# Optimization experiments

Hardware: AMD Instinct MI355X
Metric: run time of the kernel (lower is better)

The kernel has to match this reference:

```python
import jax, jax.numpy as jnp
from jax import lax
import numpy as np

B, T, UMAX, D = 32, 128, 64, 512
U1 = UMAX + 1
BLANK = D - 1  # blank=-1 -> last vocab slot
NEG = -1e30    # finite -inf surrogate (keeps logaddexp grads NaN-free)


def setup_inputs() -> dict:
    key = jax.random.key(0)
    k1, k2, k3, k4 = jax.random.split(key, 4)
    logits = jax.random.normal(k1, (B, T, U1, D), dtype=jnp.float32)
    logit_lengths = jax.random.randint(k2, (B,), T // 2, T + 1, dtype=jnp.int32)
    target_lengths = jax.random.randint(k3, (B,), UMAX // 2, UMAX + 1, dtype=jnp.int32)
    targets = jax.random.randint(k4, (B, UMAX), 0, D - 1, dtype=jnp.int32)  # never blank
    return {"logits": logits, "logit_lengths": logit_lengths,
            "target_lengths": target_lengths, "targets": targets}


def _transducer_costs(log_probs, logit_lengths, target_lengths, targets):
    """RNN-T alpha DP; costs[b] = -(alpha[T_b-1, U_b] + lp_blank[T_b-1, U_b])."""
    b, t_max, u1, d = log_probs.shape
    lp_blank = log_probs[..., BLANK]                                   # [B,T,U1]
    tgt_pad = jnp.concatenate([targets, jnp.zeros((b, 1), targets.dtype)], axis=1)  # [B,U1]
    lp_emit = jnp.take_along_axis(log_probs, tgt_pad[:, None, :, None], axis=3)[..., 0]  # [B,T,U1]
    u_idx = jnp.arange(u1)
    # emit transitions only exist for u < target_length (masks padded labels too)
    lp_emit = jnp.where(u_idx[None, None, :] < target_lengths[:, None, None], lp_emit, NEG)

    # alpha[0, u] = cumsum of emit log-probs along u
    row0 = jnp.concatenate(
        [jnp.zeros((b, 1), jnp.float32), jnp.cumsum(lp_emit[:, 0, :-1], axis=1)], axis=1)

    def row_step(prev_row, xs):
        lpb_prev, lpe = xs                      # both [B,U1]
        skip = prev_row + lpb_prev              # alpha[t-1,u] + blank(t-1,u)

        def inner(a_left, xu):
            s_u, e_um1 = xu                      # skip[:,u], lp_emit[:,t,u-1]
            a = jnp.logaddexp(s_u, a_left + e_um1)
            return a, a

        a0 = skip[:, 0]
        _, rest = lax.scan(inner, a0,
                           (jnp.moveaxis(skip[:, 1:], 1, 0),
                            jnp.moveaxis(lpe[:, :-1], 1, 0)))
        row = jnp.concatenate([a0[:, None], jnp.moveaxis(rest, 0, 1)], axis=1)
        return row, row

    xs = (jnp.moveaxis(lp_blank[:, :-1, :], 1, 0),   # blank at row t-1
          jnp.moveaxis(lp_emit[:, 1:, :], 1, 0))     # emit at row t
    _, rows = lax.scan(row_step, row0, xs)
    alpha = jnp.concatenate([row0[:, None, :], jnp.moveaxis(rows, 0, 1)], axis=1)  # [B,T,U1]

    bi = jnp.arange(b)
    tf = logit_lengths - 1
    uf = target_lengths
    return -(alpha[bi, tf, uf] + lp_blank[bi, tf, uf])


def reference(logits, logit_lengths, target_lengths, targets):
    lp = jax.nn.log_softmax(logits, axis=-1)
    return _transducer_costs(lp, logit_lengths, target_lengths, targets)
```

## Files before the change

### kernel.cpp

```cpp
#include <hip/hip_runtime.h>

#define BQ 32
#define TQ 128
#define U1Q 65
#define UMAXQ 64
#define DQ 512
#define SLAB (TQ * U1Q)
#define NCELLS (BQ * SLAB)
#define NEGQ (-1e30f)
#define L2E 1.4426950408889634f
#define LN2F 0.6931471805599453f

typedef float f4 __attribute__((ext_vector_type(4)));

__device__ __forceinline__ float logadd2(float x, float y) {
    float mx = fmaxf(x, y);
    float d  = fminf(x, y) - mx;
    return mx + log2f(1.0f + exp2f(d));
}

__global__ __launch_bounds__(512) void lse_k(const float* __restrict__ logits,
                                             const int* __restrict__ targets,
                                             const int* __restrict__ llen,
                                             const int* __restrict__ tlen,
                                             float* __restrict__ ws) {
    int wid  = (blockIdx.x * 512 + threadIdx.x) >> 6;
    int lane = threadIdx.x & 63;
    int g = lane >> 4;
    int i = lane & 15;
    int r = wid * 4 + g;

    int b = r / SLAB;
    int q = r - b * SLAB;
    int t = q / U1Q;
    int u = q - t * U1Q;
    int tl = tlen[b];
    if (t >= llen[b] || u > tl) return;

    const f4* rp = (const f4*)(logits + (size_t)r * DQ) + i;
    f4 v0 = __builtin_nontemporal_load(rp);
    f4 v1 = __builtin_nontemporal_load(rp + 16);
    f4 v2 = __builtin_nontemporal_load(rp + 32);
    f4 v3 = __builtin_nontemporal_load(rp + 48);
    f4 v4 = __builtin_nontemporal_load(rp + 64);
    f4 v5 = __builtin_nontemporal_load(rp + 80);
    f4 v6 = __builtin_nontemporal_load(rp + 96);
    f4 v7 = __builtin_nontemporal_load(rp + 112);

#define MAX4(v) fmaxf(fmaxf((v).x, (v).y), fmaxf((v).z, (v).w))
    float m = fmaxf(fmaxf(fmaxf(MAX4(v0), MAX4(v1)), fmaxf(MAX4(v2), MAX4(v3))),
                    fmaxf(fmaxf(MAX4(v4), MAX4(v5)), fmaxf(MAX4(v6), MAX4(v7))));
#pragma unroll
    for (int d = 1; d <= 8; d <<= 1) m = fmaxf(m, __shfl_xor(m, d, 64));

    float ml = m * L2E;
#define SUM4(v) (exp2f(fmaf((v).x, L2E, -ml)) + exp2f(fmaf((v).y, L2E, -ml)) + \
                 exp2f(fmaf((v).z, L2E, -ml)) + exp2f(fmaf((v).w, L2E, -ml)))
    float s = ((SUM4(v0) + SUM4(v1)) + (SUM4(v2) + SUM4(v3))) +
              ((SUM4(v4) + SUM4(v5)) + (SUM4(v6) + SUM4(v7)));
#pragma unroll
    for (int d = 1; d <= 8; d <<= 1) s += __shfl_xor(s, d, 64);

    float l2s = log2f(s);
    float* wb = ws + (size_t)b * 2 * SLAB;

    if (i == 15) wb[q] = fmaf(v7.w, L2E, -ml) - l2s;

    int tgt = targets[b * UMAXQ + (u < UMAXQ ? u : UMAXQ - 1)];
    int itgt = (tgt >> 2) & 15;
    if (i == itgt) {
        int ktgt = tgt >> 6, jt = tgt & 3;
        f4 c = v0;
        if (ktgt == 1) c = v1;
        if (ktgt == 2) c = v2;
        if (ktgt == 3) c = v3;
        if (ktgt == 4) c = v4;
        if (ktgt == 5) c = v5;
        if (ktgt == 6) c = v6;
        if (ktgt == 7) c = v7;
        float val = (jt == 0) ? c.x : ((jt == 1) ? c.y : ((jt == 2) ? c.z : c.w));
        wb[SLAB + q] = (u < tl) ? (fmaf(val, L2E, -ml) - l2s) : NEGQ;
    }
}

__global__ __launch_bounds__(512) void dp_k(const float* __restrict__ ws,
                                            const int* __restrict__ llen,
                                            const int* __restrict__ tlen,
                                            float* __restrict__ out) {
    __shared__ float S[2 * SLAB];
    int b   = blockIdx.x;
    int tid = threadIdx.x;

    int tf = llen[b] - 1;
    int uf = tlen[b];

    const f4* srcB = (const f4*)(ws + (size_t)b * 2 * SLAB);
    const f4* srcE = srcB + SLAB / 4;
    f4* dstB = (f4*)S;
    f4* dstE = (f4*)(S + SLAB);
    int nb4 = ((tf + 1) * U1Q + 3) >> 2;
    for (int idx = tid; idx < nb4; idx += 512) {
        dstB[idx] = srcB[idx];
        dstE[idx] = srcE[idx];
    }
    __syncthreads();
    if (tid >= 64) return;

    int lane = tid;
    const float* SB = S;
    const float* SE = S + SLAB;

    int kmax = tf + uf;

    float a   = (lane == 0) ? 0.0f : NEGQ;
    float a64 = NEGQ;
    int um1 = (lane > 0) ? lane - 1 : 0;

    auto LB = [&](int k) { int t = k - lane - 1; t = t < 0 ? 0 : (t > TQ - 1 ? TQ - 1 : t);
                           return SB[t * U1Q + lane]; };
    auto LE = [&](int k) { int t = k - lane;     t = t < 0 ? 0 : (t > TQ - 1 ? TQ - 1 : t);
                           return SE[t * U1Q + um1]; };
    auto LB6 = [&](int k) { int t = k - 65; t = t < 0 ? 0 : (t > TQ - 1 ? TQ - 1 : t);
                            return SB[t * U1Q + 64]; };
    auto LE6 = [&](int k) { int t = k - 64; t = t < 0 ? 0 : (t > TQ - 1 ? TQ - 1 : t);
                            return SE[t * U1Q + 63]; };

#define STEP(kk, lbv, lev, lb6v, le6v) do {                                  \
    int k_ = (kk); int t = k_ - lane;                                        \
    float A   = (t >= 1) ? (a + (lbv)) : NEGQ;                               \
    float ash = __shfl_up(a, 1, 64);                                         \
    float Bv  = (lane >= 1 && t >= 0) ? (ash + (lev)) : NEGQ;                \
    float a63 = __shfl(a, 63, 64);                                           \
    float anew = logadd2(A, Bv);                                             \
    int t64 = k_ - 64;                                                       \
    float A64 = (t64 >= 1) ? (a64 + (lb6v)) : NEGQ;                          \
    float B64 = (t64 >= 0) ? (a63 + (le6v)) : NEGQ;                          \
    a64 = (t64 >= 0) ? logadd2(A64, B64) : NEGQ;                             \
    a = anew;                                                                \
} while (0)

    float lbA = LB(1), leA = LE(1), lb6A = LB6(1), le6A = LE6(1);
    float lbB = LB(2), leB = LE(2), lb6B = LB6(2), le6B = LE6(2);
    float lbC = LB(3), leC = LE(3), lb6C = LB6(3), le6C = LE6(3);
    float lbD = LB(4), leD = LE(4), lb6D = LB6(4), le6D = LE6(4);

    int k = 1;
    for (; k + 3 <= kmax; k += 4) {
        STEP(k,     lbA, leA, lb6A, le6A); lbA = LB(k + 4); leA = LE(k + 4); lb6A = LB6(k + 4); le6A = LE6(k + 4);
        STEP(k + 1, lbB, leB, lb6B, le6B); lbB = LB(k + 5); leB = LE(k + 5); lb6B = LB6(k + 5); le6B = LE6(k + 5);
        STEP(k + 2, lbC, leC, lb6C, le6C); lbC = LB(k + 6); leC = LE(k + 6); lb6C = LB6(k + 6); le6C = LE6(k + 6);
        STEP(k + 3, lbD, leD, lb6D, le6D); lbD = LB(k + 7); leD = LE(k + 7); lb6D = LB6(k + 7); le6D = LE6(k + 7);
    }
    if (k <= kmax) { STEP(k, lbA, leA, lb6A, le6A); k++; }
    if (k <= kmax) { STEP(k, lbB, leB, lb6B, le6B); k++; }
    if (k <= kmax) { STEP(k, lbC, leC, lb6C, le6C); k++; }

    float alpha_f = (uf >= 64) ? a64 : __shfl(a, uf, 64);
    if (lane == 0) out[b] = -(alpha_f + SB[tf * U1Q + uf]) * LN2F;
}

extern "C" void kernel_launch(void* const* d_in, const int* in_sizes, int n_in,
                              void* d_out, int out_size, void* d_ws, size_t ws_size,
                              hipStream_t stream) {
    const float* logits  = (const float*)d_in[0];
    const int*   llen    = (const int*)d_in[1];
    const int*   tlen    = (const int*)d_in[2];
    const int*   targets = (const int*)d_in[3];
    float*       out     = (float*)d_out;
    float*       ws      = (float*)d_ws;

    int blocks = NCELLS / 32;
    lse_k<<<blocks, 512, 0, stream>>>(logits, targets, llen, tlen, ws);
    dp_k<<<BQ, 512, 0, stream>>>(ws, llen, tlen, out);
}
```

Before: 88.14 us.

## Compact live DP cells via prefix-sum offsets and grid-stride the softmax kernel

Adds a small prep kernel that prefix-sums the live (t,u) cell counts per batch. The log-softmax kernel then runs a fixed 1024-block grid-stride loop over only the live cells, finding each cell's batch by binary search. Previously a wave was launched for every padded cell and most returned early. The change removes idle waves and scheduling waste, at the cost of an extra kernel launch and per-cell index math.

```diff
diff --git a/kernel.cpp b/kernel.cpp
--- a/kernel.cpp
+++ b/kernel.cpp
@@ -6,7 +6,6 @@
 #define UMAXQ 64
 #define DQ 512
 #define SLAB (TQ * U1Q)
-#define NCELLS (BQ * SLAB)
 #define NEGQ (-1e30f)
 #define L2E 1.4426950408889634f
 #define LN2F 0.6931471805599453f
@@ -19,67 +18,97 @@
     return mx + log2f(1.0f + exp2f(d));
 }
 
+__global__ __launch_bounds__(64) void prep_k(const int* __restrict__ llen,
+                                             const int* __restrict__ tlen,
+                                             int* __restrict__ offt) {
+    int lane = threadIdx.x;
+    int v = (lane < BQ) ? llen[lane] * (tlen[lane] + 1) : 0;
+    int p = v;
+#pragma unroll
+    for (int d = 1; d <= 16; d <<= 1) { int o = __shfl_up(p, d, 64); if (lane >= d) p += o; }
+    if (lane < BQ) offt[lane + 1] = p;
+    if (lane == 0) offt[0] = 0;
+}
+
 __global__ __launch_bounds__(512) void lse_k(const float* __restrict__ logits,
                                              const int* __restrict__ targets,
-                                             const int* __restrict__ llen,
                                              const int* __restrict__ tlen,
+                                             const int* __restrict__ offt,
                                              float* __restrict__ ws) {
-    int wid  = (blockIdx.x * 512 + threadIdx.x) >> 6;
-    int lane = threadIdx.x & 63;
+    __shared__ int Soff[BQ + 1];
+    __shared__ int Stl[BQ];
+    int tid = threadIdx.x;
+    if (tid < BQ + 1) Soff[tid] = offt[tid];
+    if (tid < BQ)     Stl[tid]  = tlen[tid];
+    __syncthreads();
+    int total = Soff[BQ];
+
+    int lane = tid & 63;
     int g = lane >> 4;
     int i = lane & 15;
-    int r = wid * 4 + g;
-
-    int b = r / SLAB;
-    int q = r - b * SLAB;
-    int t = q / U1Q;
-    int u = q - t * U1Q;
-    int tl = tlen[b];
-    if (t >= llen[b] || u > tl) return;
-
-    const f4* rp = (const f4*)(logits + (size_t)r * DQ) + i;
-    f4 v0 = __builtin_nontemporal_load(rp);
-    f4 v1 = __builtin_nontemporal_load(rp + 16);
-    f4 v2 = __builtin_nontemporal_load(rp + 32);
-    f4 v3 = __builtin_nontemporal_load(rp + 48);
-    f4 v4 = __builtin_nontemporal_load(rp + 64);
-    f4 v5 = __builtin_nontemporal_load(rp + 80);
-    f4 v6 = __builtin_nontemporal_load(rp + 96);
-    f4 v7 = __builtin_nontemporal_load(rp + 112);
+    int wid = blockIdx.x * 8 + (tid >> 6);
+    int stride = gridDim.x * 8 * 4;
+
+    for (int base = wid * 4; base < total; base += stride) {
+        int ar = base + g;
+        bool alive = (ar < total);
+        if (!alive) ar = total - 1;
+
+        int lo = 0, hi = BQ;
+#pragma unroll
+        for (int it = 0; it < 5; ++it) { int mid = (lo + hi) >> 1; if (ar >= Soff[mid]) lo = mid; else hi = mid; }
+        int b = lo;
+        int tl = Stl[b];
+        int P = tl + 1;
+        int local = ar - Soff[b];
+        int t = local / P;
+        int u = local - t * P;
+        int q = t * U1Q + u;
+
+        const f4* rp = (const f4*)(logits + ((size_t)b * SLAB + q) * DQ) + i;
+        f4 v0 = __builtin_nontemporal_load(rp);
+        f4 v1 = __builtin_nontemporal_load(rp + 16);
+        f4 v2 = __builtin_nontemporal_load(rp + 32);
+        f4 v3 = __builtin_nontemporal_load(rp + 48);
+        f4 v4 = __builtin_nontemporal_load(rp + 64);
+        f4 v5 = __builtin_nontemporal_load(rp + 80);
+        f4 v6 = __builtin_nontemporal_load(rp + 96);
+        f4 v7 = __builtin_nontemporal_load(rp + 112);
 
 #define MAX4(v) fmaxf(fmaxf((v).x, (v).y), fmaxf((v).z, (v).w))
-    float m = fmaxf(fmaxf(fmaxf(MAX4(v0), MAX4(v1)), fmaxf(MAX4(v2), MAX4(v3))),
-                    fmaxf(fmaxf(MAX4(v4), MAX4(v5)), fmaxf(MAX4(v6), MAX4(v7))));
-#pragma unroll
-    for (int d = 1; d <= 8; d <<= 1) m = fmaxf(m, __shfl_xor(m, d, 64));
-
-    float ml = m * L2E;
+        float m = fmaxf(fmaxf(fmaxf(MAX4(v0), MAX4(v1)), fmaxf(MAX4(v2), MAX4(v3))),
+                        fmaxf(fmaxf(MAX4(v4), MAX4(v5)), fmaxf(MAX4(v6), MAX4(v7))));
+#pragma unroll
+        for (int d = 1; d <= 8; d <<= 1) m = fmaxf(m, __shfl_xor(m, d, 64));
+
+        float ml = m * L2E;
 #define SUM4(v) (exp2f(fmaf((v).x, L2E, -ml)) + exp2f(fmaf((v).y, L2E, -ml)) + \
                  exp2f(fmaf((v).z, L2E, -ml)) + exp2f(fmaf((v).w, L2E, -ml)))
-    float s = ((SUM4(v0) + SUM4(v1)) + (SUM4(v2) + SUM4(v3))) +
-              ((SUM4(v4) + SUM4(v5)) + (SUM4(v6) + SUM4(v7)));
-#pragma unroll
-    for (int d = 1; d <= 8; d <<= 1) s += __shfl_xor(s, d, 64);
-
-    float l2s = log2f(s);
-    float* wb = ws + (size_t)b * 2 * SLAB;
-
-    if (i == 15) wb[q] = fmaf(v7.w, L2E, -ml) - l2s;
-
-    int tgt = targets[b * UMAXQ + (u < UMAXQ ? u : UMAXQ - 1)];
-    int itgt = (tgt >> 2) & 15;
-    if (i == itgt) {
-        int ktgt = tgt >> 6, jt = tgt & 3;
-        f4 c = v0;
-        if (ktgt == 1) c = v1;
-        if (ktgt == 2) c = v2;
-        if (ktgt == 3) c = v3;
-        if (ktgt == 4) c = v4;
-        if (ktgt == 5) c = v5;
-        if (ktgt == 6) c = v6;
-        if (ktgt == 7) c = v7;
-        float val = (jt == 0) ? c.x : ((jt == 1) ? c.y : ((jt == 2) ? c.z : c.w));
-        wb[SLAB + q] = (u < tl) ? (fmaf(val, L2E, -ml) - l2s) : NEGQ;
+        float s = ((SUM4(v0) + SUM4(v1)) + (SUM4(v2) + SUM4(v3))) +
+                  ((SUM4(v4) + SUM4(v5)) + (SUM4(v6) + SUM4(v7)));
+#pragma unroll
+        for (int d = 1; d <= 8; d <<= 1) s += __shfl_xor(s, d, 64);
+
+        float l2s = log2f(s);
+        float* wb = ws + (size_t)b * 2 * SLAB;
+
+        if (alive && i == 15) wb[q] = fmaf(v7.w, L2E, -ml) - l2s;
+
+        int tgt = targets[b * UMAXQ + (u < UMAXQ ? u : UMAXQ - 1)];
+        int itgt = (tgt >> 2) & 15;
+        if (alive && i == itgt) {
+            int ktgt = tgt >> 6, jt = tgt & 3;
+            f4 c = v0;
+            if (ktgt == 1) c = v1;
+            if (ktgt == 2) c = v2;
+            if (ktgt == 3) c = v3;
+            if (ktgt == 4) c = v4;
+            if (ktgt == 5) c = v5;
+            if (ktgt == 6) c = v6;
+            if (ktgt == 7) c = v7;
+            float val = (jt == 0) ? c.x : ((jt == 1) ? c.y : ((jt == 2) ? c.z : c.w));
+            wb[SLAB + q] = (u < tl) ? (fmaf(val, L2E, -ml) - l2s) : NEGQ;
+        }
     }
 }
 
@@ -168,8 +197,9 @@
     const int*   targets = (const int*)d_in[3];
     float*       out     = (float*)d_out;
     float*       ws      = (float*)d_ws;
-
-    int blocks = NCELLS / 32;
-    lse_k<<<blocks, 512, 0, stream>>>(logits, targets, llen, tlen, ws);
+    int*         offt    = (int*)(ws + (size_t)2 * SLAB * BQ);
+
+    prep_k<<<1, 64, 0, stream>>>(llen, tlen, offt);
+    lse_k<<<1024, 512, 0, stream>>>(logits, targets, tlen, offt, ws);
     dp_k<<<BQ, 512, 0, stream>>>(ws, llen, tlen, out);
 }
```

After: 97.34 us. 1.1x slower.
